# Optimization experiments

Hardware: AMD Instinct MI355X
Metric: run time of the kernel (lower is better)

## Reference

```python
import jax, jax.numpy as jnp
import numpy as np

BN_EPS = 1e-5


def setup_inputs() -> dict:
    key = jax.random.key(0)
    ks = jax.random.split(key, 12)
    B, N, S, D1, D2 = 2, 16384, 4096, 128, 256
    C1, C2 = 256, 128  # mlp channels
    return {
        "xyz1": jax.random.normal(ks[0], (B, 3, N), dtype=jnp.float32),
        "xyz2": jax.random.normal(ks[1], (B, 3, S), dtype=jnp.float32),
        "points1": jax.random.normal(ks[2], (B, D1, N), dtype=jnp.float32),
        "points2": jax.random.normal(ks[3], (B, D2, S), dtype=jnp.float32),
        "w1": jax.random.normal(ks[4], (D1 + D2, C1), dtype=jnp.float32) * 0.05,
        "b1": jax.random.normal(ks[5], (C1,), dtype=jnp.float32) * 0.05,
        "g1": jax.random.uniform(ks[6], (C1,), dtype=jnp.float32, minval=0.5, maxval=1.5),
        "beta1": jax.random.normal(ks[7], (C1,), dtype=jnp.float32) * 0.05,
        "w2": jax.random.normal(ks[8], (C1, C2), dtype=jnp.float32) * 0.05,
        "b2": jax.random.normal(ks[9], (C2,), dtype=jnp.float32) * 0.05,
        "g2": jax.random.uniform(ks[10], (C2,), dtype=jnp.float32, minval=0.5, maxval=1.5),
        "beta2": jax.random.normal(ks[11], (C2,), dtype=jnp.float32) * 0.05,
    }


def _conv_bn_relu(x, W, b, g, beta):
    # 1x1 Conv1d == per-point matmul; BatchNorm1d training-mode stats over (B, N).
    y = x @ W + b                              # [B, N, Cout]
    mu = jnp.mean(y, axis=(0, 1))
    var = jnp.var(y, axis=(0, 1))              # biased variance, matches torch BN
    y = g * (y - mu) * jax.lax.rsqrt(var + BN_EPS) + beta
    return jax.nn.relu(y)


def reference(xyz1, xyz2, points1, points2, w1, b1, g1, beta1, w2, b2, g2, beta2):
    x1 = jnp.transpose(xyz1, (0, 2, 1))        # [B, N, 3]
    x2 = jnp.transpose(xyz2, (0, 2, 1))        # [B, S, 3]
    p2 = jnp.transpose(points2, (0, 2, 1))     # [B, S, D2]

    # squared pairwise distance [B, N, S], clamped at 0
    d = (jnp.sum(x1 ** 2, axis=-1, keepdims=True)
         - 2.0 * jnp.einsum('bnc,bsc->bns', x1, x2)
         + jnp.sum(x2 ** 2, axis=-1)[:, None, :])
    d = jnp.maximum(d, 0.0)

    # 3 nearest neighbors (ascending smallest distances) -- same math as full sort + slice
    neg_d3, idx = jax.lax.top_k(-d, 3)         # [B, N, 3]
    d3 = jnp.maximum(-neg_d3, 1e-6)
    recip = 1.0 / d3
    w = recip / jnp.maximum(jnp.sum(recip, axis=-1, keepdims=True), 1e-6)

    nb = jax.vmap(lambda p, i: p[i])(p2, idx)  # [B, N, 3, D2]
    interp = jnp.sum(nb * w[..., None], axis=2)
    interp = jnp.nan_to_num(interp, nan=0.0, posinf=0.0, neginf=0.0)

    p1 = jnp.transpose(points1, (0, 2, 1))     # [B, N, D1]
    x = jnp.concatenate([p1, interp], axis=-1) # [B, N, D1+D2]

    x = _conv_bn_relu(x, w1, b1, g1, beta1)
    x = _conv_bn_relu(x, w2, b2, g2, beta2)
    x = jnp.nan_to_num(x, nan=0.0, posinf=0.0, neginf=0.0)
    return jnp.transpose(x, (0, 2, 1))         # [B, C2, N]
```

## Files before the change

kernel.cpp:

```cpp
#include <hip/hip_runtime.h>

#define B_   2
#define N_   16384
#define S_   4096
#define D1_  128
#define D2_  256
#define C1_  256
#define C2_  128
#define M_   (B_ * N_)

typedef __bf16 bf16_t;
typedef bf16_t bf16x8 __attribute__((ext_vector_type(8)));
typedef bf16_t bf16x4 __attribute__((ext_vector_type(4)));
typedef float  f32x4  __attribute__((ext_vector_type(4)));

__device__ __forceinline__ void gload16(const void* g, void* l) {
  __builtin_amdgcn_global_load_lds(
      (const __attribute__((address_space(1))) void*)g,
      (__attribute__((address_space(3))) void*)l, 16, 0, 0);
}

__device__ __forceinline__ float med3f(float a, float b, float c) {
  float d;
  asm("v_med3_f32 %0, %1, %2, %3" : "=v"(d) : "v"(a), "v"(b), "v"(c));
  return d;
}

__global__ __launch_bounds__(256) void setup_k(const float* __restrict__ points2,
                                               const float* __restrict__ points1,
                                               const float* __restrict__ w1,
                                               const float* __restrict__ w2,
                                               const float* __restrict__ xyz2,
                                               float* __restrict__ p2t,
                                               bf16_t* __restrict__ X,
                                               bf16_t* __restrict__ w1t,
                                               bf16_t* __restrict__ w2t,
                                               float4* __restrict__ c4) {
  __shared__ float tile[32][33];
  int bi = blockIdx.x, t = threadIdx.x;
  int tx = t & 31, ty = t >> 5;
  if (bi < 2048) {
    int b = bi >> 10, rest = bi & 1023;
    int s0 = (rest & 127) * 32, c0 = (rest >> 7) * 32;
    const float* src = points2 + (size_t)b * D2_ * S_;
#pragma unroll
    for (int k = 0; k < 4; ++k)
      tile[ty + k * 8][tx] = src[(size_t)(c0 + ty + k * 8) * S_ + s0 + tx];
    __syncthreads();
    float* dst = p2t + (size_t)b * S_ * D2_;
#pragma unroll
    for (int k = 0; k < 4; ++k)
      dst[(size_t)(s0 + ty + k * 8) * D2_ + c0 + tx] = tile[tx][ty + k * 8];
  } else if (bi < 6144) {
    int bj = bi - 2048;
    int b = bj >> 11, rest = bj & 2047;
    int n0 = (rest & 511) * 32, c0 = (rest >> 9) * 32;
    const float* src = points1 + (size_t)b * D1_ * N_;
#pragma unroll
    for (int k = 0; k < 4; ++k)
      tile[ty + k * 8][tx] = src[(size_t)(c0 + ty + k * 8) * N_ + n0 + tx];
    __syncthreads();
#pragma unroll
    for (int k = 0; k < 4; ++k)
      X[(size_t)(b * N_ + n0 + ty + k * 8) * 384 + c0 + tx] = (bf16_t)tile[tx][ty + k * 8];
  } else {
    int i = (bi - 6144) * 256 + t;
    if (i < C1_ * 384) {
      int n = i / 384, k = i % 384;
      w1t[i] = (bf16_t)w1[(size_t)k * C1_ + n];
    } else if (i < C1_ * 384 + C2_ * C1_) {
      int j = i - C1_ * 384;
      int n = j / C1_, k = j % C1_;
      w2t[j] = (bf16_t)w2[(size_t)k * C2_ + n];
    } else {
      int j = i - (C1_ * 384 + C2_ * C1_);
      if (j < B_ * S_) {
        int b = j >> 12, s = j & (S_ - 1);
        const float* X2p = xyz2 + (size_t)b * 3 * S_;
        float x = X2p[s], y = X2p[S_ + s], z = X2p[2 * S_ + s];
        c4[j] = make_float4(-2.f * x, -2.f * y, -2.f * z, x * x + y * y + z * z);
      }
    }
  }
}

__global__ __launch_bounds__(512, 8) void knn_k(const float* __restrict__ xyz1,
                                                const float4* __restrict__ c4,
                                                const float* __restrict__ p2t,
                                                bf16_t* __restrict__ X) {
  __shared__ float4 cbuf[1024];
  __shared__ float  T3V[2][3][32];
  __shared__ int    T3I[2][3][32];
  __shared__ float  QWs[32][3];
  __shared__ int    QIs[32][3];
  int t = threadIdx.x, l = t & 63, w = t >> 6;
  int q = l & 31, h = l >> 5;
  int s = w * 2 + h;
  int b  = blockIdx.x >> 9;
  int nb = (blockIdx.x & 511) * 32;
  int n  = nb + q;
  const float* X1 = xyz1 + (size_t)b * 3 * N_;
  float ax = X1[n], ay = X1[N_ + n], az = X1[2 * N_ + n];
  float negp = -(ax * ax + ay * ay + az * az);
  const float4* cb = c4 + (size_t)b * S_;
  float m0 = 3e38f, m1 = 3e38f, m2 = 3e38f;
  int   j0 = 0, j1 = 0, j2 = 0;
  for (int r = 0; r < 4; ++r) {
    __syncthreads();
    gload16(cb + r * 1024 + t,       (char*)cbuf + (size_t)t * 16);
    gload16(cb + r * 1024 + t + 512, (char*)cbuf + (size_t)(t + 512) * 16);
    __syncthreads();
    const float4* cs = cbuf + s * 64;
    int base = r * 1024 + s * 64;
#pragma unroll 4
    for (int i = 0; i < 64; ++i) {
      float4 c = cs[i];
      float v = c.w;
      v = fmaf(az, c.z, v);
      v = fmaf(ay, c.y, v);
      v = fmaf(ax, c.x, v);
      v = fmaxf(v, negp);
      int idx = base + i;
      bool b0 = v < m0, b1 = v < m1, b2 = v < m2;
      float nm0 = fminf(v, m0);
      float nm1 = med3f(m0, v, m1);
      float nm2 = med3f(m1, v, m2);
      j2 = b1 ? j1 : (b2 ? idx : j2);
      j1 = b0 ? j0 : (b1 ? idx : j1);
      j0 = b0 ? idx : j0;
      m0 = nm0; m1 = nm1; m2 = nm2;
    }
  }
  __syncthreads();
  float* SV = (float*)cbuf;
  int*   SI = (int*)cbuf + 1536;
  SV[(s * 3 + 0) * 32 + q] = m0;  SV[(s * 3 + 1) * 32 + q] = m1;  SV[(s * 3 + 2) * 32 + q] = m2;
  SI[(s * 3 + 0) * 32 + q] = j0;  SI[(s * 3 + 1) * 32 + q] = j1;  SI[(s * 3 + 2) * 32 + q] = j2;
  __syncthreads();
  if (t < 64) {
    int th = t >> 5, tq = t & 31;
    float M0 = 3e38f, M1 = 3e38f, M2 = 3e38f;
    int   a0 = 0, a1 = 0, a2 = 0;
    for (int s2 = th * 8; s2 < th * 8 + 8; ++s2)
#pragma unroll
      for (int k = 0; k < 3; ++k) {
        float v = SV[(s2 * 3 + k) * 32 + tq];
        int  ix = SI[(s2 * 3 + k) * 32 + tq];
        bool b0 = v < M0, b1 = v < M1, b2 = v < M2;
        float nm0 = fminf(v, M0);
        float nm1 = med3f(M0, v, M1);
        float nm2 = med3f(M1, v, M2);
        a2 = b1 ? a1 : (b2 ? ix : a2);
        a1 = b0 ? a0 : (b1 ? ix : a1);
        a0 = b0 ? ix : a0;
        M0 = nm0; M1 = nm1; M2 = nm2;
      }
    T3V[th][0][tq] = M0; T3V[th][1][tq] = M1; T3V[th][2][tq] = M2;
    T3I[th][0][tq] = a0; T3I[th][1][tq] = a1; T3I[th][2][tq] = a2;
  }
  __syncthreads();
  if (t < 32) {
    float M0 = T3V[0][0][t], M1 = T3V[0][1][t], M2 = T3V[0][2][t];
    int   a0 = T3I[0][0][t], a1 = T3I[0][1][t], a2 = T3I[0][2][t];
#pragma unroll
    for (int k = 0; k < 3; ++k) {
      float v = T3V[1][k][t];
      int  ix = T3I[1][k][t];
      bool b0 = v < M0, b1 = v < M1, b2 = v < M2;
      float nm0 = fminf(v, M0);
      float nm1 = med3f(M0, v, M1);
      float nm2 = med3f(M1, v, M2);
      a2 = b1 ? a1 : (b2 ? ix : a2);
      a1 = b0 ? a0 : (b1 ? ix : a1);
      a0 = b0 ? ix : a0;
      M0 = nm0; M1 = nm1; M2 = nm2;
    }
    float p  = -negp;
    float d0 = fmaxf(p + M0, 1e-6f);
    float d1 = fmaxf(p + M1, 1e-6f);
    float d2 = fmaxf(p + M2, 1e-6f);
    float r0 = 1.f / d0, r1 = 1.f / d1, r2 = 1.f / d2;
    float dn = fmaxf(r0 + r1 + r2, 1e-6f);
    QWs[t][0] = r0 / dn;  QWs[t][1] = r1 / dn;  QWs[t][2] = r2 / dn;
    QIs[t][0] = a0;       QIs[t][1] = a1;       QIs[t][2] = a2;
  }
  __syncthreads();
  int gq = t >> 4, c0 = (t & 15) * 16;
  float w0 = QWs[gq][0], w1 = QWs[gq][1], w2 = QWs[gq][2];
  int   i0 = QIs[gq][0], i1 = QIs[gq][1], i2 = QIs[gq][2];
  const float* pb = p2t + (size_t)b * S_ * D2_;
  bf16_t* xo = X + ((size_t)(b * N_ + nb + gq)) * 384 + 128 + c0;
#pragma unroll
  for (int u = 0; u < 4; ++u) {
    float4 A  = *(const float4*)(pb + (size_t)i0 * D2_ + c0 + u * 4);
    float4 Bv = *(const float4*)(pb + (size_t)i1 * D2_ + c0 + u * 4);
    float4 Cv = *(const float4*)(pb + (size_t)i2 * D2_ + c0 + u * 4);
    bf16x4 o;
    o[0] = (bf16_t)(w0 * A.x + w1 * Bv.x + w2 * Cv.x);
    o[1] = (bf16_t)(w0 * A.y + w1 * Bv.y + w2 * Cv.y);
    o[2] = (bf16_t)(w0 * A.z + w1 * Bv.z + w2 * Cv.z);
    o[3] = (bf16_t)(w0 * A.w + w1 * Bv.w + w2 * Cv.w);
    *(bf16x4*)&xo[u * 4] = o;
  }
}

__global__ __launch_bounds__(256) void gemm1_k(const bf16_t* __restrict__ A,
                                               const bf16_t* __restrict__ Bt,
                                               const float* __restrict__ bias,
                                               bf16_t* __restrict__ Y,
                                               float* __restrict__ st) {
  const int K = 384;
  __shared__ bf16_t As[128 * 32];
  __shared__ bf16_t Bs[128 * 32];
  int tid = threadIdx.x, lane = tid & 63, w = tid >> 6;
  int wr = w >> 1, wc = w & 1;
  int m0 = blockIdx.x * 128, n0 = blockIdx.y * 128;
  int e0 = (w * 2 + 0) * 512 + lane * 8;
  int e1 = (w * 2 + 1) * 512 + lane * 8;
  int ra0 = e0 >> 5, ca0 = e0 & 31;
  int ra1 = e1 >> 5, ca1 = e1 & 31;
  f32x4 acc[4][4];
  f32x4 z = {0.f, 0.f, 0.f, 0.f};
#pragma unroll
  for (int i = 0; i < 4; ++i)
#pragma unroll
    for (int j = 0; j < 4; ++j) acc[i][j] = z;
  for (int k0 = 0; k0 < K; k0 += 32) {
    __syncthreads();
    gload16(A + (size_t)(m0 + ra0) * K + k0 + ca0, &As[e0]);
    gload16(A + (size_t)(m0 + ra1) * K + k0 + ca1, &As[e1]);
    gload16(Bt + (size_t)(n0 + ra0) * K + k0 + ca0, &Bs[e0]);
    gload16(Bt + (size_t)(n0 + ra1) * K + k0 + ca1, &Bs[e1]);
    __syncthreads();
    bf16x8 af[4], bfr[4];
    int arow = wr * 64 + (lane & 15);
    int brow = wc * 64 + (lane & 15);
    int kc = 8 * (lane >> 4);
#pragma unroll
    for (int i = 0; i < 4; ++i) af[i]  = *(const bf16x8*)&As[(arow + i * 16) * 32 + kc];
#pragma unroll
    for (int j = 0; j < 4; ++j) bfr[j] = *(const bf16x8*)&Bs[(brow + j * 16) * 32 + kc];
#pragma unroll
    for (int i = 0; i < 4; ++i)
#pragma unroll
      for (int j = 0; j < 4; ++j)
        acc[i][j] = __builtin_amdgcn_mfma_f32_16x16x32_bf16(af[i], bfr[j], acc[i][j], 0, 0, 0);
  }
#pragma unroll
  for (int j = 0; j < 4; ++j) {
    int col = n0 + wc * 64 + j * 16 + (lane & 15);
    float bv = bias[col];
    float sj = 0.f, ssj = 0.f;
#pragma unroll
    for (int i = 0; i < 4; ++i) {
      int r = m0 + wr * 64 + i * 16 + ((lane >> 4) << 2);
#pragma unroll
      for (int q = 0; q < 4; ++q) {
        float y = acc[i][j][q] + bv;
        Y[(size_t)(r + q) * C1_ + col] = (bf16_t)y;
        sj += y; ssj += y * y;
      }
    }
    sj  += __shfl_xor(sj, 16);  sj  += __shfl_xor(sj, 32);
    ssj += __shfl_xor(ssj, 16); ssj += __shfl_xor(ssj, 32);
    if ((lane >> 4) == 0) {
      atomicAdd(&st[col], sj);
      atomicAdd(&st[C1_ + col], ssj);
    }
  }
}

__global__ __launch_bounds__(256) void bn1apply_k(const bf16_t* __restrict__ Y,
                                                  const float* __restrict__ st,
                                                  const float* __restrict__ g,
                                                  const float* __restrict__ be,
                                                  bf16_t* __restrict__ X2) {
  __shared__ float sa[256], sb[256];
  int t = threadIdx.x;
  {
    const float invM = 1.f / (float)M_;
    float mu  = st[t] * invM;
    float var = fmaxf(st[C1_ + t] * invM - mu * mu, 0.f);
    float a = g[t] * rsqrtf(var + 1e-5f);
    sa[t] = a;
    sb[t] = be[t] - mu * a;
  }
  __syncthreads();
  int cc = (t & 31) * 8;
  float a[8], s[8];
#pragma unroll
  for (int u = 0; u < 8; ++u) { a[u] = sa[cc + u]; s[u] = sb[cc + u]; }
  int r0 = blockIdx.x * 64 + (t >> 5);
  for (int it = 0; it < 8; ++it) {
    int r = r0 + it * 8;
    bf16x8 v = *(const bf16x8*)&Y[(size_t)r * C1_ + cc];
    bf16x8 o;
#pragma unroll
    for (int u = 0; u < 8; ++u) {
      float f = (float)v[u];
      f = fmaxf(a[u] * f + s[u], 0.f);
      o[u] = (bf16_t)f;
    }
    *(bf16x8*)&X2[(size_t)r * C1_ + cc] = o;
  }
}

__global__ __launch_bounds__(256) void gemm2_k(const bf16_t* __restrict__ A,
                                               const bf16_t* __restrict__ Bt,
                                               const float* __restrict__ bias,
                                               float* __restrict__ OUT,
                                               float* __restrict__ st) {
  const int K = 256;
  __shared__ bf16_t As[128 * 32];
  __shared__ bf16_t Bs[128 * 32];
  int tid = threadIdx.x, lane = tid & 63, w = tid >> 6;
  int wr = w >> 1, wc = w & 1;
  int m0 = blockIdx.x * 128;
  int e0 = (w * 2 + 0) * 512 + lane * 8;
  int e1 = (w * 2 + 1) * 512 + lane * 8;
  int ra0 = e0 >> 5, ca0 = e0 & 31;
  int ra1 = e1 >> 5, ca1 = e1 & 31;
  f32x4 acc[4][4];
  f32x4 z = {0.f, 0.f, 0.f, 0.f};
#pragma unroll
  for (int i = 0; i < 4; ++i)
#pragma unroll
    for (int j = 0; j < 4; ++j) acc[i][j] = z;
  for (int k0 = 0; k0 < K; k0 += 32) {
    __syncthreads();
    gload16(A + (size_t)(m0 + ra0) * K + k0 + ca0, &As[e0]);
    gload16(A + (size_t)(m0 + ra1) * K + k0 + ca1, &As[e1]);
    gload16(Bt + (size_t)ra0 * K + k0 + ca0, &Bs[e0]);
    gload16(Bt + (size_t)ra1 * K + k0 + ca1, &Bs[e1]);
    __syncthreads();
    bf16x8 af[4], bfr[4];
    int arow = wr * 64 + (lane & 15);
    int brow = wc * 64 + (lane & 15);
    int kc = 8 * (lane >> 4);
#pragma unroll
    for (int i = 0; i < 4; ++i) af[i]  = *(const bf16x8*)&As[(arow + i * 16) * 32 + kc];
#pragma unroll
    for (int j = 0; j < 4; ++j) bfr[j] = *(const bf16x8*)&Bs[(brow + j * 16) * 32 + kc];
#pragma unroll
    for (int i = 0; i < 4; ++i)
#pragma unroll
      for (int j = 0; j < 4; ++j)
        acc[i][j] = __builtin_amdgcn_mfma_f32_16x16x32_bf16(af[i], bfr[j], acc[i][j], 0, 0, 0);
  }
#pragma unroll
  for (int j = 0; j < 4; ++j) {
    int col = wc * 64 + j * 16 + (lane & 15);
    float bv = bias[col];
    float sj = 0.f, ssj = 0.f;
#pragma unroll
    for (int i = 0; i < 4; ++i) {
      int r  = m0 + wr * 64 + i * 16 + ((lane >> 4) << 2);
      int bb = r >> 14, n = r & (N_ - 1);
      f32x4 v = acc[i][j];
#pragma unroll
      for (int q = 0; q < 4; ++q) {
        v[q] += bv;
        sj += v[q]; ssj += v[q] * v[q];
      }
      *(f32x4*)&OUT[((size_t)(bb * C2_ + col)) * N_ + n] = v;
    }
    sj  += __shfl_xor(sj, 16);  sj  += __shfl_xor(sj, 32);
    ssj += __shfl_xor(ssj, 16); ssj += __shfl_xor(ssj, 32);
    if ((lane >> 4) == 0) {
      atomicAdd(&st[col], sj);
      atomicAdd(&st[C2_ + col], ssj);
    }
  }
}

__global__ __launch_bounds__(256) void bn2apply_k(float* __restrict__ OUT,
                                                  const float* __restrict__ st,
                                                  const float* __restrict__ g,
                                                  const float* __restrict__ be) {
  __shared__ float ab[2];
  int t = threadIdx.x;
  int c = (blockIdx.x >> 4) & 127;
  if (t == 0) {
    const float invM = 1.f / (float)M_;
    float mu  = st[c] * invM;
    float var = fmaxf(st[C2_ + c] * invM - mu * mu, 0.f);
    float a = g[c] * rsqrtf(var + 1e-5f);
    ab[0] = a;
    ab[1] = be[c] - mu * a;
  }
  __syncthreads();
  float a = ab[0], s = ab[1];
  size_t i4 = (size_t)blockIdx.x * 256 + t;
  f32x4 v = *(f32x4*)&OUT[i4 * 4];
#pragma unroll
  for (int u = 0; u < 4; ++u) v[u] = fmaxf(a * v[u] + s, 0.f);
  *(f32x4*)&OUT[i4 * 4] = v;
}

extern "C" void kernel_launch(void* const* d_in, const int* in_sizes, int n_in,
                              void* d_out, int out_size, void* d_ws, size_t ws_size,
                              hipStream_t stream) {
  const float* xyz1    = (const float*)d_in[0];
  const float* xyz2    = (const float*)d_in[1];
  const float* points1 = (const float*)d_in[2];
  const float* points2 = (const float*)d_in[3];
  const float* w1      = (const float*)d_in[4];
  const float* b1      = (const float*)d_in[5];
  const float* g1      = (const float*)d_in[6];
  const float* beta1   = (const float*)d_in[7];
  const float* w2      = (const float*)d_in[8];
  const float* b2      = (const float*)d_in[9];
  const float* g2      = (const float*)d_in[10];
  const float* beta2   = (const float*)d_in[11];
  float* out = (float*)d_out;

  char* p = (char*)d_ws;
  size_t off = 0;
  bf16_t* w1t = (bf16_t*)(p + off); off += (size_t)C1_ * 384 * 2;
  bf16_t* w2t = (bf16_t*)(p + off); off += (size_t)C2_ * C1_ * 2;
  float*  p2t = (float*)(p + off);  off += (size_t)B_ * S_ * D2_ * 4;
  bf16_t* X   = (bf16_t*)(p + off); off += (size_t)M_ * 384 * 2;
  bf16_t* Y1  = (bf16_t*)(p + off); off += (size_t)M_ * C1_ * 2;
  bf16_t* X2  = (bf16_t*)(p + off); off += (size_t)M_ * C1_ * 2;
  float4* C4  = (float4*)(p + off); off += (size_t)B_ * S_ * 16;
  float*  ST1 = (float*)(p + off);  off += 2048;
  float*  ST2 = (float*)(p + off);  off += 1024;

  hipMemsetAsync(ST1, 0, 3072, stream);

  setup_k<<<6688, 256, 0, stream>>>(points2, points1, w1, w2, xyz2, p2t, X, w1t, w2t, C4);
  knn_k<<<1024, 512, 0, stream>>>(xyz1, C4, p2t, X);
  gemm1_k<<<dim3(M_ / 128, 2), 256, 0, stream>>>(X, w1t, b1, Y1, ST1);
  bn1apply_k<<<512, 256, 0, stream>>>(Y1, ST1, g1, beta1, X2);
  gemm2_k<<<M_ / 128, 256, 0, stream>>>(X2, w2t, b2, out, ST2);
  bn2apply_k<<<4096, 256, 0, stream>>>(out, ST2, g2, beta2);
}
```

Before: 144.0 us.

## Precompute points2·W1b per source point, fuse BN applies, drop interpolation buffer

Because the interpolation and the first matmul are both linear, the change computes G = points2ᵀ·W1[128:] once per source point (S rows instead of N). gemm1 then reduces to K=128 and adds a weighted gather of three G rows in its epilogue. KNN now writes only indices and weights. BN1 apply is folded into gemm2's A-tile load, and BN2 apply is folded into gemm2 through a grid-wide atomic barrier, so two elementwise kernels go away. The risks are a possible deadlock if not all 256 blocks can be co-resident, precision changes from the bf16 points2 and the reordered sums, and uncoalesced G gathers in the gemm1 epilogue.

After: 172.9 us. +20.1%, slower.

```diff
diff --git a/kernel.cpp b/kernel.cpp
--- a/kernel.cpp
+++ b/kernel.cpp
@@ -11,7 +11,6 @@
 
 typedef __bf16 bf16_t;
 typedef bf16_t bf16x8 __attribute__((ext_vector_type(8)));
-typedef bf16_t bf16x4 __attribute__((ext_vector_type(4)));
 typedef float  f32x4  __attribute__((ext_vector_type(4)));
 
 __device__ __forceinline__ void gload16(const void* g, void* l) {
@@ -20,20 +19,27 @@
       (__attribute__((address_space(3))) void*)l, 16, 0, 0);
 }
 
-__device__ __forceinline__ float med3f(float a, float b, float c) {
-  float d;
-  asm("v_med3_f32 %0, %1, %2, %3" : "=v"(d) : "v"(a), "v"(b), "v"(c));
-  return d;
-}
+#define INSERT3(v, ix)                                                   \
+  {                                                                      \
+    bool b0_ = (v) < m0, b1_ = (v) < m1, b2_ = (v) < m2;                 \
+    float nm0 = fminf((v), m0);                                          \
+    float nm1 = fminf(fmaxf((v), m0), m1);                               \
+    float nm2 = fminf(fmaxf((v), m1), m2);                               \
+    j2 = b1_ ? j1 : (b2_ ? (ix) : j2);                                   \
+    j1 = b0_ ? j0 : (b1_ ? (ix) : j1);                                   \
+    j0 = b0_ ? (ix) : j0;                                                \
+    m0 = nm0; m1 = nm1; m2 = nm2;                                        \
+  }
 
 __global__ __launch_bounds__(256) void setup_k(const float* __restrict__ points2,
                                                const float* __restrict__ points1,
                                                const float* __restrict__ w1,
                                                const float* __restrict__ w2,
                                                const float* __restrict__ xyz2,
-                                               float* __restrict__ p2t,
-                                               bf16_t* __restrict__ X,
-                                               bf16_t* __restrict__ w1t,
+                                               bf16_t* __restrict__ p2tb,
+                                               bf16_t* __restrict__ Xp1,
+                                               bf16_t* __restrict__ w1at,
+                                               bf16_t* __restrict__ w1bt,
                                                bf16_t* __restrict__ w2t,
                                                float4* __restrict__ c4) {
   __shared__ float tile[32][33];
@@ -47,10 +53,10 @@
     for (int k = 0; k < 4; ++k)
       tile[ty + k * 8][tx] = src[(size_t)(c0 + ty + k * 8) * S_ + s0 + tx];
     __syncthreads();
-    float* dst = p2t + (size_t)b * S_ * D2_;
+    bf16_t* dst = p2tb + (size_t)b * S_ * D2_;
 #pragma unroll
     for (int k = 0; k < 4; ++k)
-      dst[(size_t)(s0 + ty + k * 8) * D2_ + c0 + tx] = tile[tx][ty + k * 8];
+      dst[(size_t)(s0 + ty + k * 8) * D2_ + c0 + tx] = (bf16_t)tile[tx][ty + k * 8];
   } else if (bi < 6144) {
     int bj = bi - 2048;
     int b = bj >> 11, rest = bj & 2047;
@@ -62,18 +68,22 @@
     __syncthreads();
 #pragma unroll
     for (int k = 0; k < 4; ++k)
-      X[(size_t)(b * N_ + n0 + ty + k * 8) * 384 + c0 + tx] = (bf16_t)tile[tx][ty + k * 8];
+      Xp1[(size_t)(b * N_ + n0 + ty + k * 8) * 128 + c0 + tx] = (bf16_t)tile[tx][ty + k * 8];
   } else {
     int i = (bi - 6144) * 256 + t;
-    if (i < C1_ * 384) {
-      int n = i / 384, k = i % 384;
-      w1t[i] = (bf16_t)w1[(size_t)k * C1_ + n];
-    } else if (i < C1_ * 384 + C2_ * C1_) {
-      int j = i - C1_ * 384;
-      int n = j / C1_, k = j % C1_;
+    if (i < 32768) {
+      int n = i >> 7, k = i & 127;
+      w1at[i] = (bf16_t)w1[(size_t)k * C1_ + n];
+    } else if (i < 98304) {
+      int j = i - 32768;
+      int n = j >> 8, k = j & 255;
+      w1bt[j] = (bf16_t)w1[(size_t)(128 + k) * C1_ + n];
+    } else if (i < 131072) {
+      int j = i - 98304;
+      int n = j >> 8, k = j & 255;
       w2t[j] = (bf16_t)w2[(size_t)k * C2_ + n];
     } else {
-      int j = i - (C1_ * 384 + C2_ * C1_);
+      int j = i - 131072;
       if (j < B_ * S_) {
         int b = j >> 12, s = j & (S_ - 1);
         const float* X2p = xyz2 + (size_t)b * 3 * S_;
@@ -84,15 +94,69 @@
   }
 }
 
+__global__ __launch_bounds__(256) void gemmG_k(const bf16_t* __restrict__ A,
+                                               const bf16_t* __restrict__ Bt,
+                                               float* __restrict__ G) {
+  const int K = 256;
+  __shared__ bf16_t As[128 * 32];
+  __shared__ bf16_t Bs[128 * 32];
+  int tid = threadIdx.x, lane = tid & 63, w = tid >> 6;
+  int wr = w >> 1, wc = w & 1;
+  int z  = blockIdx.z;
+  int m0 = blockIdx.x * 128, n0 = blockIdx.y * 128;
+  const bf16_t* Ab = A + (size_t)z * S_ * 256;
+  float* Gb = G + (size_t)z * S_ * 256;
+  int e0 = (w * 2 + 0) * 512 + lane * 8;
+  int e1 = (w * 2 + 1) * 512 + lane * 8;
+  int ra0 = e0 >> 5, ca0 = e0 & 31;
+  int ra1 = e1 >> 5, ca1 = e1 & 31;
+  f32x4 acc[4][4];
+  f32x4 zv = {0.f, 0.f, 0.f, 0.f};
+#pragma unroll
+  for (int i = 0; i < 4; ++i)
+#pragma unroll
+    for (int j = 0; j < 4; ++j) acc[i][j] = zv;
+  for (int k0 = 0; k0 < K; k0 += 32) {
+    __syncthreads();
+    gload16(Ab + (size_t)(m0 + ra0) * K + k0 + ca0, &As[e0]);
+    gload16(Ab + (size_t)(m0 + ra1) * K + k0 + ca1, &As[e1]);
+    gload16(Bt + (size_t)(n0 + ra0) * K + k0 + ca0, &Bs[e0]);
+    gload16(Bt + (size_t)(n0 + ra1) * K + k0 + ca1, &Bs[e1]);
+    __syncthreads();
+    bf16x8 af[4], bfr[4];
+    int arow = wr * 64 + (lane & 15);
+    int brow = wc * 64 + (lane & 15);
+    int kc = 8 * (lane >> 4);
+#pragma unroll
+    for (int i = 0; i < 4; ++i) af[i]  = *(const bf16x8*)&As[(arow + i * 16) * 32 + kc];
+#pragma unroll
+    for (int j = 0; j < 4; ++j) bfr[j] = *(const bf16x8*)&Bs[(brow + j * 16) * 32 + kc];
+#pragma unroll
+    for (int i = 0; i < 4; ++i)
+#pragma unroll
+      for (int j = 0; j < 4; ++j)
+        acc[i][j] = __builtin_amdgcn_mfma_f32_16x16x32_bf16(af[i], bfr[j], acc[i][j], 0, 0, 0);
+  }
+#pragma unroll
+  for (int j = 0; j < 4; ++j) {
+    int col = n0 + wc * 64 + j * 16 + (lane & 15);
+#pragma unroll
+    for (int i = 0; i < 4; ++i) {
+      int r = m0 + wr * 64 + i * 16 + ((lane >> 4) << 2);
+#pragma unroll
+      for (int q = 0; q < 4; ++q)
+        Gb[(size_t)(r + q) * 256 + col] = acc[i][j][q];
+    }
+  }
+}
+
 __global__ __launch_bounds__(512, 8) void knn_k(const float* __restrict__ xyz1,
                                                 const float4* __restrict__ c4,
-                                                const float* __restrict__ p2t,
-                                                bf16_t* __restrict__ X) {
+                                                float* __restrict__ kw,
+                                                int* __restrict__ ki) {
   __shared__ float4 cbuf[1024];
   __shared__ float  T3V[2][3][32];
   __shared__ int    T3I[2][3][32];
-  __shared__ float  QWs[32][3];
-  __shared__ int    QIs[32][3];
   int t = threadIdx.x, l = t & 63, w = t >> 6;
   int q = l & 31, h = l >> 5;
   int s = w * 2 + h;
@@ -101,7 +165,7 @@
   int n  = nb + q;
   const float* X1 = xyz1 + (size_t)b * 3 * N_;
   float ax = X1[n], ay = X1[N_ + n], az = X1[2 * N_ + n];
-  float negp = -(ax * ax + ay * ay + az * az);
+  float p = ax * ax + ay * ay + az * az;
   const float4* cb = c4 + (size_t)b * S_;
   float m0 = 3e38f, m1 = 3e38f, m2 = 3e38f;
   int   j0 = 0, j1 = 0, j2 = 0;
@@ -112,23 +176,15 @@
     __syncthreads();
     const float4* cs = cbuf + s * 64;
     int base = r * 1024 + s * 64;
-#pragma unroll 4
+#pragma unroll 8
     for (int i = 0; i < 64; ++i) {
       float4 c = cs[i];
       float v = c.w;
       v = fmaf(az, c.z, v);
       v = fmaf(ay, c.y, v);
       v = fmaf(ax, c.x, v);
-      v = fmaxf(v, negp);
       int idx = base + i;
-      bool b0 = v < m0, b1 = v < m1, b2 = v < m2;
-      float nm0 = fminf(v, m0);
-      float nm1 = med3f(m0, v, m1);
-      float nm2 = med3f(m1, v, m2);
-      j2 = b1 ? j1 : (b2 ? idx : j2);
-      j1 = b0 ? j0 : (b1 ? idx : j1);
-      j0 = b0 ? idx : j0;
-      m0 = nm0; m1 = nm1; m2 = nm2;
+      INSERT3(v, idx);
     }
   }
   __syncthreads();
@@ -141,75 +197,51 @@
     int th = t >> 5, tq = t & 31;
     float M0 = 3e38f, M1 = 3e38f, M2 = 3e38f;
     int   a0 = 0, a1 = 0, a2 = 0;
-    for (int s2 = th * 8; s2 < th * 8 + 8; ++s2)
-#pragma unroll
-      for (int k = 0; k < 3; ++k) {
-        float v = SV[(s2 * 3 + k) * 32 + tq];
-        int  ix = SI[(s2 * 3 + k) * 32 + tq];
-        bool b0 = v < M0, b1 = v < M1, b2 = v < M2;
-        float nm0 = fminf(v, M0);
-        float nm1 = med3f(M0, v, M1);
-        float nm2 = med3f(M1, v, M2);
-        a2 = b1 ? a1 : (b2 ? ix : a2);
-        a1 = b0 ? a0 : (b1 ? ix : a1);
-        a0 = b0 ? ix : a0;
-        M0 = nm0; M1 = nm1; M2 = nm2;
-      }
+    {
+      float m0 = M0, m1 = M1, m2 = M2;
+      int j0 = a0, j1 = a1, j2 = a2;
+      for (int s2 = th * 8; s2 < th * 8 + 8; ++s2)
+#pragma unroll
+        for (int k = 0; k < 3; ++k) {
+          float v = SV[(s2 * 3 + k) * 32 + tq];
+          int  ix = SI[(s2 * 3 + k) * 32 + tq];
+          INSERT3(v, ix);
+        }
+      M0 = m0; M1 = m1; M2 = m2; a0 = j0; a1 = j1; a2 = j2;
+    }
     T3V[th][0][tq] = M0; T3V[th][1][tq] = M1; T3V[th][2][tq] = M2;
     T3I[th][0][tq] = a0; T3I[th][1][tq] = a1; T3I[th][2][tq] = a2;
   }
   __syncthreads();
   if (t < 32) {
-    float M0 = T3V[0][0][t], M1 = T3V[0][1][t], M2 = T3V[0][2][t];
-    int   a0 = T3I[0][0][t], a1 = T3I[0][1][t], a2 = T3I[0][2][t];
+    float m0 = T3V[0][0][t], m1 = T3V[0][1][t], m2 = T3V[0][2][t];
+    int   j0 = T3I[0][0][t], j1 = T3I[0][1][t], j2 = T3I[0][2][t];
 #pragma unroll
     for (int k = 0; k < 3; ++k) {
       float v = T3V[1][k][t];
       int  ix = T3I[1][k][t];
-      bool b0 = v < M0, b1 = v < M1, b2 = v < M2;
-      float nm0 = fminf(v, M0);
-      float nm1 = med3f(M0, v, M1);
-      float nm2 = med3f(M1, v, M2);
-      a2 = b1 ? a1 : (b2 ? ix : a2);
-      a1 = b0 ? a0 : (b1 ? ix : a1);
-      a0 = b0 ? ix : a0;
-      M0 = nm0; M1 = nm1; M2 = nm2;
-    }
-    float p  = -negp;
-    float d0 = fmaxf(p + M0, 1e-6f);
-    float d1 = fmaxf(p + M1, 1e-6f);
-    float d2 = fmaxf(p + M2, 1e-6f);
+      INSERT3(v, ix);
+    }
+    float d0 = fmaxf(p + m0, 1e-6f);
+    float d1 = fmaxf(p + m1, 1e-6f);
+    float d2 = fmaxf(p + m2, 1e-6f);
     float r0 = 1.f / d0, r1 = 1.f / d1, r2 = 1.f / d2;
     float dn = fmaxf(r0 + r1 + r2, 1e-6f);
-    QWs[t][0] = r0 / dn;  QWs[t][1] = r1 / dn;  QWs[t][2] = r2 / dn;
-    QIs[t][0] = a0;       QIs[t][1] = a1;       QIs[t][2] = a2;
-  }
-  __syncthreads();
-  int gq = t >> 4, c0 = (t & 15) * 16;
-  float w0 = QWs[gq][0], w1 = QWs[gq][1], w2 = QWs[gq][2];
-  int   i0 = QIs[gq][0], i1 = QIs[gq][1], i2 = QIs[gq][2];
-  const float* pb = p2t + (size_t)b * S_ * D2_;
-  bf16_t* xo = X + ((size_t)(b * N_ + nb + gq)) * 384 + 128 + c0;
-#pragma unroll
-  for (int u = 0; u < 4; ++u) {
-    float4 A  = *(const float4*)(pb + (size_t)i0 * D2_ + c0 + u * 4);
-    float4 Bv = *(const float4*)(pb + (size_t)i1 * D2_ + c0 + u * 4);
-    float4 Cv = *(const float4*)(pb + (size_t)i2 * D2_ + c0 + u * 4);
-    bf16x4 o;
-    o[0] = (bf16_t)(w0 * A.x + w1 * Bv.x + w2 * Cv.x);
-    o[1] = (bf16_t)(w0 * A.y + w1 * Bv.y + w2 * Cv.y);
-    o[2] = (bf16_t)(w0 * A.z + w1 * Bv.z + w2 * Cv.z);
-    o[3] = (bf16_t)(w0 * A.w + w1 * Bv.w + w2 * Cv.w);
-    *(bf16x4*)&xo[u * 4] = o;
+    size_t rr = (size_t)b * N_ + n;
+    kw[rr * 3 + 0] = r0 / dn;  kw[rr * 3 + 1] = r1 / dn;  kw[rr * 3 + 2] = r2 / dn;
+    ki[rr * 3 + 0] = j0;       ki[rr * 3 + 1] = j1;       ki[rr * 3 + 2] = j2;
   }
 }
 
 __global__ __launch_bounds__(256) void gemm1_k(const bf16_t* __restrict__ A,
                                                const bf16_t* __restrict__ Bt,
                                                const float* __restrict__ bias,
+                                               const float* __restrict__ G,
+                                               const float* __restrict__ KW,
+                                               const int* __restrict__ KI,
                                                bf16_t* __restrict__ Y,
                                                float* __restrict__ st) {
-  const int K = 384;
+  const int K = 128;
   __shared__ bf16_t As[128 * 32];
   __shared__ bf16_t Bs[128 * 32];
   int tid = threadIdx.x, lane = tid & 63, w = tid >> 6;
@@ -246,76 +278,83 @@
       for (int j = 0; j < 4; ++j)
         acc[i][j] = __builtin_amdgcn_mfma_f32_16x16x32_bf16(af[i], bfr[j], acc[i][j], 0, 0, 0);
   }
+  __syncthreads();
+  float* kwls = (float*)As;
+  int*   kils = ((int*)As) + 384;
+  if (tid < 128) {
+    int r = m0 + tid;
+    kwls[tid * 3 + 0] = KW[(size_t)r * 3 + 0];
+    kwls[tid * 3 + 1] = KW[(size_t)r * 3 + 1];
+    kwls[tid * 3 + 2] = KW[(size_t)r * 3 + 2];
+    kils[tid * 3 + 0] = KI[(size_t)r * 3 + 0];
+    kils[tid * 3 + 1] = KI[(size_t)r * 3 + 1];
+    kils[tid * 3 + 2] = KI[(size_t)r * 3 + 2];
+  }
+  __syncthreads();
+  int bb = m0 >> 14;
+  const float* Gb = G + (size_t)bb * S_ * 256;
+  float sjv[4]  = {0.f, 0.f, 0.f, 0.f};
+  float ssjv[4] = {0.f, 0.f, 0.f, 0.f};
+#pragma unroll
+  for (int i = 0; i < 4; ++i) {
+#pragma unroll
+    for (int qq = 0; qq < 4; ++qq) {
+      int rl = wr * 64 + i * 16 + ((lane >> 4) << 2) + qq;
+      float w0 = kwls[rl * 3 + 0], w1v = kwls[rl * 3 + 1], w2v = kwls[rl * 3 + 2];
+      const float* g0 = Gb + (size_t)kils[rl * 3 + 0] * 256;
+      const float* g1 = Gb + (size_t)kils[rl * 3 + 1] * 256;
+      const float* g2 = Gb + (size_t)kils[rl * 3 + 2] * 256;
+      int r = m0 + rl;
+#pragma unroll
+      for (int j = 0; j < 4; ++j) {
+        int col = n0 + wc * 64 + j * 16 + (lane & 15);
+        float y = acc[i][j][qq] + bias[col]
+                + w0 * g0[col] + w1v * g1[col] + w2v * g2[col];
+        Y[(size_t)r * C1_ + col] = (bf16_t)y;
+        sjv[j] += y;  ssjv[j] += y * y;
+      }
+    }
+  }
 #pragma unroll
   for (int j = 0; j < 4; ++j) {
-    int col = n0 + wc * 64 + j * 16 + (lane & 15);
-    float bv = bias[col];
-    float sj = 0.f, ssj = 0.f;
-#pragma unroll
-    for (int i = 0; i < 4; ++i) {
-      int r = m0 + wr * 64 + i * 16 + ((lane >> 4) << 2);
-#pragma unroll
-      for (int q = 0; q < 4; ++q) {
-        float y = acc[i][j][q] + bv;
-        Y[(size_t)(r + q) * C1_ + col] = (bf16_t)y;
-        sj += y; ssj += y * y;
-      }
-    }
+    float sj = sjv[j], ssj = ssjv[j];
     sj  += __shfl_xor(sj, 16);  sj  += __shfl_xor(sj, 32);
     ssj += __shfl_xor(ssj, 16); ssj += __shfl_xor(ssj, 32);
     if ((lane >> 4) == 0) {
+      int col = n0 + wc * 64 + j * 16 + (lane & 15);
       atomicAdd(&st[col], sj);
       atomicAdd(&st[C1_ + col], ssj);
     }
   }
 }
 
-__global__ __launch_bounds__(256) void bn1apply_k(const bf16_t* __restrict__ Y,
-                                                  const float* __restrict__ st,
-                                                  const float* __restrict__ g,
-                                                  const float* __restrict__ be,
-                                                  bf16_t* __restrict__ X2) {
-  __shared__ float sa[256], sb[256];
-  int t = threadIdx.x;
-  {
-    const float invM = 1.f / (float)M_;
-    float mu  = st[t] * invM;
-    float var = fmaxf(st[C1_ + t] * invM - mu * mu, 0.f);
-    float a = g[t] * rsqrtf(var + 1e-5f);
-    sa[t] = a;
-    sb[t] = be[t] - mu * a;
-  }
-  __syncthreads();
-  int cc = (t & 31) * 8;
-  float a[8], s[8];
-#pragma unroll
-  for (int u = 0; u < 8; ++u) { a[u] = sa[cc + u]; s[u] = sb[cc + u]; }
-  int r0 = blockIdx.x * 64 + (t >> 5);
-  for (int it = 0; it < 8; ++it) {
-    int r = r0 + it * 8;
-    bf16x8 v = *(const bf16x8*)&Y[(size_t)r * C1_ + cc];
-    bf16x8 o;
-#pragma unroll
-    for (int u = 0; u < 8; ++u) {
-      float f = (float)v[u];
-      f = fmaxf(a[u] * f + s[u], 0.f);
-      o[u] = (bf16_t)f;
-    }
-    *(bf16x8*)&X2[(size_t)r * C1_ + cc] = o;
-  }
-}
-
-__global__ __launch_bounds__(256) void gemm2_k(const bf16_t* __restrict__ A,
-                                               const bf16_t* __restrict__ Bt,
-                                               const float* __restrict__ bias,
-                                               float* __restrict__ OUT,
-                                               float* __restrict__ st) {
+__global__ __launch_bounds__(256, 2) void gemm2_k(const bf16_t* __restrict__ Y1,
+                                                  const bf16_t* __restrict__ Bt,
+                                                  const float* __restrict__ bias,
+                                                  const float* __restrict__ st1,
+                                                  const float* __restrict__ g1v,
+                                                  const float* __restrict__ be1,
+                                                  float* __restrict__ OUT,
+                                                  float* __restrict__ st2,
+                                                  const float* __restrict__ g2v,
+                                                  const float* __restrict__ be2,
+                                                  int* __restrict__ cnt) {
   const int K = 256;
   __shared__ bf16_t As[128 * 32];
   __shared__ bf16_t Bs[128 * 32];
+  __shared__ float sa1[C1_], sb1[C1_];
+  __shared__ float a2s[C2_], b2s[C2_];
   int tid = threadIdx.x, lane = tid & 63, w = tid >> 6;
   int wr = w >> 1, wc = w & 1;
   int m0 = blockIdx.x * 128;
+  {
+    const float invM = 1.f / (float)M_;
+    float mu  = st1[tid] * invM;
+    float var = fmaxf(st1[C1_ + tid] * invM - mu * mu, 0.f);
+    float a = g1v[tid] * rsqrtf(var + 1e-5f);
+    sa1[tid] = a;
+    sb1[tid] = be1[tid] - mu * a;
+  }
   int e0 = (w * 2 + 0) * 512 + lane * 8;
   int e1 = (w * 2 + 1) * 512 + lane * 8;
   int ra0 = e0 >> 5, ca0 = e0 & 31;
@@ -326,10 +365,23 @@
   for (int i = 0; i < 4; ++i)
 #pragma unroll
     for (int j = 0; j < 4; ++j) acc[i][j] = z;
+  __syncthreads();
   for (int k0 = 0; k0 < K; k0 += 32) {
-    __syncthreads();
-    gload16(A + (size_t)(m0 + ra0) * K + k0 + ca0, &As[e0]);
-    gload16(A + (size_t)(m0 + ra1) * K + k0 + ca1, &As[e1]);
+    if (k0) __syncthreads();
+    bf16x8 va0 = *(const bf16x8*)&Y1[(size_t)(m0 + ra0) * C1_ + k0 + ca0];
+    bf16x8 va1 = *(const bf16x8*)&Y1[(size_t)(m0 + ra1) * C1_ + k0 + ca1];
+    bf16x8 oa0, oa1;
+#pragma unroll
+    for (int u = 0; u < 8; ++u) {
+      float f0 = (float)va0[u];
+      float f1 = (float)va1[u];
+      f0 = fmaxf(f0 * sa1[k0 + ca0 + u] + sb1[k0 + ca0 + u], 0.f);
+      f1 = fmaxf(f1 * sa1[k0 + ca1 + u] + sb1[k0 + ca1 + u], 0.f);
+      oa0[u] = (bf16_t)f0;
+      oa1[u] = (bf16_t)f1;
+    }
+    *(bf16x8*)&As[e0] = oa0;
+    *(bf16x8*)&As[e1] = oa1;
     gload16(Bt + (size_t)ra0 * K + k0 + ca0, &Bs[e0]);
     gload16(Bt + (size_t)ra1 * K + k0 + ca1, &Bs[e1]);
     __syncthreads();
@@ -367,34 +419,40 @@
     sj  += __shfl_xor(sj, 16);  sj  += __shfl_xor(sj, 32);
     ssj += __shfl_xor(ssj, 16); ssj += __shfl_xor(ssj, 32);
     if ((lane >> 4) == 0) {
-      atomicAdd(&st[col], sj);
-      atomicAdd(&st[C2_ + col], ssj);
-    }
-  }
-}
-
-__global__ __launch_bounds__(256) void bn2apply_k(float* __restrict__ OUT,
-                                                  const float* __restrict__ st,
-                                                  const float* __restrict__ g,
-                                                  const float* __restrict__ be) {
-  __shared__ float ab[2];
-  int t = threadIdx.x;
-  int c = (blockIdx.x >> 4) & 127;
-  if (t == 0) {
+      atomicAdd(&st2[col], sj);
+      atomicAdd(&st2[C2_ + col], ssj);
+    }
+  }
+  __syncthreads();
+  if (tid == 0) {
+    __threadfence();
+    atomicAdd(cnt, 1);
+    while (__hip_atomic_load(cnt, __ATOMIC_ACQUIRE, __HIP_MEMORY_SCOPE_AGENT) < (int)gridDim.x)
+      __builtin_amdgcn_s_sleep(8);
+  }
+  __syncthreads();
+  if (tid < C2_) {
+    float s  = __hip_atomic_load(&st2[tid],        __ATOMIC_RELAXED, __HIP_MEMORY_SCOPE_AGENT);
+    float ss = __hip_atomic_load(&st2[C2_ + tid],  __ATOMIC_RELAXED, __HIP_MEMORY_SCOPE_AGENT);
     const float invM = 1.f / (float)M_;
-    float mu  = st[c] * invM;
-    float var = fmaxf(st[C2_ + c] * invM - mu * mu, 0.f);
-    float a = g[c] * rsqrtf(var + 1e-5f);
-    ab[0] = a;
-    ab[1] = be[c] - mu * a;
-  }
-  __syncthreads();
-  float a = ab[0], s = ab[1];
-  size_t i4 = (size_t)blockIdx.x * 256 + t;
-  f32x4 v = *(f32x4*)&OUT[i4 * 4];
-#pragma unroll
-  for (int u = 0; u < 4; ++u) v[u] = fmaxf(a * v[u] + s, 0.f);
-  *(f32x4*)&OUT[i4 * 4] = v;
+    float mu  = s * invM;
+    float var = fmaxf(ss * invM - mu * mu, 0.f);
+    float a = g2v[tid] * rsqrtf(var + 1e-5f);
+    a2s[tid] = a;
+    b2s[tid] = be2[tid] - mu * a;
+  }
+  __syncthreads();
+  int bb = m0 >> 14, ng = m0 & (N_ - 1);
+  int c = tid >> 1, half = tid & 1;
+  float a = a2s[c], sft = b2s[c];
+  float* pr = OUT + ((size_t)(bb * C2_ + c)) * N_ + ng + half * 64;
+#pragma unroll
+  for (int u2 = 0; u2 < 16; ++u2) {
+    f32x4 v = *(f32x4*)&pr[u2 * 4];
+#pragma unroll
+    for (int u = 0; u < 4; ++u) v[u] = fmaxf(a * v[u] + sft, 0.f);
+    *(f32x4*)&pr[u2 * 4] = v;
+  }
 }
 
 extern "C" void kernel_launch(void* const* d_in, const int* in_sizes, int n_in,
@@ -416,22 +474,27 @@
 
   char* p = (char*)d_ws;
   size_t off = 0;
-  bf16_t* w1t = (bf16_t*)(p + off); off += (size_t)C1_ * 384 * 2;
-  bf16_t* w2t = (bf16_t*)(p + off); off += (size_t)C2_ * C1_ * 2;
-  float*  p2t = (float*)(p + off);  off += (size_t)B_ * S_ * D2_ * 4;
-  bf16_t* X   = (bf16_t*)(p + off); off += (size_t)M_ * 384 * 2;
-  bf16_t* Y1  = (bf16_t*)(p + off); off += (size_t)M_ * C1_ * 2;
-  bf16_t* X2  = (bf16_t*)(p + off); off += (size_t)M_ * C1_ * 2;
-  float4* C4  = (float4*)(p + off); off += (size_t)B_ * S_ * 16;
-  float*  ST1 = (float*)(p + off);  off += 2048;
-  float*  ST2 = (float*)(p + off);  off += 1024;
-
-  hipMemsetAsync(ST1, 0, 3072, stream);
-
-  setup_k<<<6688, 256, 0, stream>>>(points2, points1, w1, w2, xyz2, p2t, X, w1t, w2t, C4);
-  knn_k<<<1024, 512, 0, stream>>>(xyz1, C4, p2t, X);
-  gemm1_k<<<dim3(M_ / 128, 2), 256, 0, stream>>>(X, w1t, b1, Y1, ST1);
-  bn1apply_k<<<512, 256, 0, stream>>>(Y1, ST1, g1, beta1, X2);
-  gemm2_k<<<M_ / 128, 256, 0, stream>>>(X2, w2t, b2, out, ST2);
-  bn2apply_k<<<4096, 256, 0, stream>>>(out, ST2, g2, beta2);
-}
+  bf16_t* Xp1  = (bf16_t*)(p + off); off += (size_t)M_ * 128 * 2;
+  bf16_t* P2TB = (bf16_t*)(p + off); off += (size_t)B_ * S_ * D2_ * 2;
+  bf16_t* W1AT = (bf16_t*)(p + off); off += (size_t)C1_ * 128 * 2;
+  bf16_t* W1BT = (bf16_t*)(p + off); off += (size_t)C1_ * 256 * 2;
+  bf16_t* W2T  = (bf16_t*)(p + off); off += (size_t)C2_ * C1_ * 2;
+  float4* C4   = (float4*)(p + off); off += (size_t)B_ * S_ * 16;
+  float*  G    = (float*)(p + off);  off += (size_t)B_ * S_ * 256 * 4;
+  bf16_t* Y1   = (bf16_t*)(p + off); off += (size_t)M_ * C1_ * 2;
+  float*  KW   = (float*)(p + off);  off += (size_t)M_ * 3 * 4;
+  int*    KI   = (int*)(p + off);    off += (size_t)M_ * 3 * 4;
+  float*  ST1  = (float*)(p + off);  off += 2048;
+  float*  ST2  = (float*)(p + off);  off += 1024;
+  int*    CNT  = (int*)(p + off);    off += 16;
+
+  hipMemsetAsync(ST1, 0, 2048 + 1024 + 16, stream);
+
+  setup_k<<<6688, 256, 0, stream>>>(points2, points1, w1, w2, xyz2,
+                                    P2TB, Xp1, W1AT, W1BT, W2T, C4);
+  gemmG_k<<<dim3(S_ / 128, 2, B_), 256, 0, stream>>>(P2TB, W1BT, G);
+  knn_k<<<1024, 512, 0, stream>>>(xyz1, C4, KW, KI);
+  gemm1_k<<<dim3(M_ / 128, 2), 256, 0, stream>>>(Xp1, W1AT, b1, G, KW, KI, Y1, ST1);
+  gemm2_k<<<M_ / 128, 256, 0, stream>>>(Y1, W2T, b2, ST1, g1, beta1,
+                                        out, ST2, g2, beta2, CNT);
+}
```
